# Performance work log

Measured on AMD Instinct MI355X. Metric: run time of the kernel, lower is better.

Reference implementation:

```python
import jax, jax.numpy as jnp
import numpy as np

NUM_SAMPLES = 4_194_304  # 2**22 samples (~87s @ 48kHz) -> memory-bound streaming IIR


def setup_inputs() -> dict:
    key = jax.random.key(0)
    k1, k2 = jax.random.split(key)
    # [attack, decay, filter_lp, filter_hp, gain]; uniform(0,1) is in the valid clamped range
    parameters = jax.random.uniform(k1, (5,), dtype=jnp.float32)
    noise = jax.random.normal(k2, (NUM_SAMPLES,), dtype=jnp.float32)
    return {"parameters": parameters, "noise": noise}


def _one_pole_lowpass(x, c):
    # y[n] = (1 - c) * x[n] + c * y[n-1]
    def step(y_prev, xn):
        y = (1.0 - c) * xn + c * y_prev
        return y, y
    _, y = jax.lax.scan(step, jnp.zeros((), x.dtype), x)
    return y


def _one_pole_highpass(x, c):
    # y[n] = c * (y[n-1] + x[n] - x[n-1])
    dx = jnp.concatenate([x[:1], x[1:] - x[:-1]])
    def step(y_prev, d):
        y = c * (y_prev + d)
        return y, y
    _, y = jax.lax.scan(step, jnp.zeros((), x.dtype), dx)
    return y


def reference(parameters, noise):
    attack = jnp.clip(parameters[0], 1e-7, None)
    decay = jnp.clip(parameters[1], 1e-7, None)
    filter_lp = jnp.clip(parameters[2], 1e-7, 0.99)
    filter_hp = jnp.clip(parameters[3], 1e-7, 0.99)
    gain = jnp.clip(parameters[4], 1e-7, None)

    n = noise.shape[0]
    t = jnp.linspace(0.0, 1.0, n, dtype=noise.dtype)  # matches registered 'time' buffer
    # exponential attack/decay envelope
    envelope = (1.0 - jnp.exp(-t / attack)) * jnp.exp(-t / decay)

    filtered = _one_pole_lowpass(noise, filter_lp)
    filtered = _one_pole_highpass(filtered, filter_hp)
    return filtered * envelope * gain
```

## Files before the change

kernel.cpp:

```cpp
#include <hip/hip_runtime.h>
#include <math.h>


#define BLOCK 256
#define CHUNK 16
#define SAMP  (BLOCK * CHUNK)
#define ESTG_CAP 4096

typedef float vfloat4 __attribute__((ext_vector_type(4)));
typedef float vfloat2 __attribute__((ext_vector_type(2)));

__device__ float Est_g[ESTG_CAP];

struct Op { float a, w, b; };
__device__ __forceinline__ Op opmul(Op A, Op B) {
    Op C;
    C.a = A.a * B.a;
    C.w = fmaf(A.w, B.a, A.b * B.w);
    C.b = A.b * B.b;
    return C;
}

template<bool EMIT>
__global__ __launch_bounds__(BLOCK, 4) void ng_kernel(
    const float* __restrict__ params,
    const float* __restrict__ noise,
    float* __restrict__ out,
    float* __restrict__ EstArg,
    int n)
{
    __shared__ float swy[4], swz[4], ry[4], rz[4];

    float* __restrict__ Est = EstArg ? EstArg : Est_g;

    const int tid  = threadIdx.x;
    const int lane = tid & 63;
    const int wid  = tid >> 6;
    const int b    = blockIdx.x;
    const int g0   = b * SAMP + tid * CHUNK;

    const float a   = fminf(fmaxf(params[2], 1e-7f), 0.99f);
    const float bb  = fminf(fmaxf(params[3], 1e-7f), 0.99f);
    const float omc = 1.0f - a;

    int nt = 0;
    vfloat2 Ev[4] = {{0.f,0.f},{0.f,0.f},{0.f,0.f},{0.f,0.f}};
    if (EMIT) {
        int em = b - 1 - tid;
        nt = (em >= 0) ? ((em >> 8) + 1) : 0;
        #pragma unroll
        for (int j = 0; j < 4; ++j) {
            if (j < nt) {
                int u = b - 1 - tid - (j << 8);
                Ev[j] = *(const vfloat2*)(Est + 2 * u);
            }
        }
    }

    vfloat4 xq[4];
    if (g0 + CHUNK <= n) {
        #pragma unroll
        for (int q = 0; q < 4; ++q)
            xq[q] = *(const vfloat4*)(noise + g0 + 4 * q);
    } else {
        #pragma unroll
        for (int q = 0; q < 4; ++q) {
            #pragma unroll
            for (int c = 0; c < 4; ++c) {
                int g = g0 + 4 * q + c;
                xq[q][c] = (g < n) ? noise[g] : 0.0f;
            }
        }
    }

    float yv = 0.0f, zv = 0.0f;
    #pragma unroll
    for (int j = 0; j < CHUNK; ++j) {
        float x  = xq[j >> 2][j & 3];
        float yn = fmaf(a, yv, omc * x);
        zv = bb * (zv + (yn - yv));
        yv = yn;
    }

    Op m1 = { a, bb * (a - 1.0f), bb };
    Op m2 = opmul(m1, m1), m4 = opmul(m2, m2), m8 = opmul(m4, m4);
    Op P  = opmul(m8, m8);
    Op O  = { 1.0f, 0.0f, 1.0f };
    float cy = yv, cz = zv;
    #pragma unroll
    for (int k = 0; k < 6; ++k) {
        if (EMIT && ((lane >> k) & 1)) O = opmul(P, O);
        int d = 1 << k;
        float py = __shfl_up(cy, d, 64);
        float pz = __shfl_up(cz, d, 64);
        if (lane >= d) {
            cy = fmaf(P.a, py, cy);
            cz = fmaf(P.w, py, fmaf(P.b, pz, cz));
        }
        P = opmul(P, P);
    }
    if (lane == 63) { swy[wid] = cy; swz[wid] = cz; }
    __syncthreads();

    float pry = 0.0f, prz = 0.0f;
    for (int u = 0; u < wid; ++u) {
        float ny = fmaf(P.a, pry, swy[u]);
        float nz = fmaf(P.w, pry, fmaf(P.b, prz, swz[u]));
        pry = ny; prz = nz;
    }

    if (!EMIT) {
        if (tid == 255) {
            vfloat2 e;
            e.x = fmaf(P.a, pry, cy);
            e.y = fmaf(P.w, pry, fmaf(P.b, prz, cz));
            *(vfloat2*)(Est + 2 * b) = e;
        }
        return;
    }

    float ey = __shfl_up(cy, 1, 64);
    float ez = __shfl_up(cz, 1, 64);
    if (lane == 0) { ey = 0.0f; ez = 0.0f; }

    Op R2 = opmul(P, P);
    Op Q  = opmul(R2, R2);
    Op Ot = { 1.0f, 0.0f, 1.0f };
    Op cur = Q;
    #pragma unroll
    for (int k = 0; k < 8; ++k) {
        if ((tid >> k) & 1) Ot = opmul(cur, Ot);
        cur = opmul(cur, cur);
    }
    float Hy = 0.0f, Hz = 0.0f;
    for (int j = nt - 1; j >= 4; --j) {
        int u = b - 1 - tid - (j << 8);
        vfloat2 e = *(const vfloat2*)(Est + 2 * u);
        float t = fmaf(cur.a, Hy, e.x);
        Hz = fmaf(cur.w, Hy, fmaf(cur.b, Hz, e.y));
        Hy = t;
    }
    #pragma unroll
    for (int j = 3; j >= 0; --j) {
        if (j < nt) {
            float t = fmaf(cur.a, Hy, Ev[j].x);
            Hz = fmaf(cur.w, Hy, fmaf(cur.b, Hz, Ev[j].y));
            Hy = t;
        }
    }
    float vy = Ot.a * Hy;
    float vz = fmaf(Ot.w, Hy, Ot.b * Hz);
    #pragma unroll
    for (int d = 1; d < 64; d <<= 1) {
        vy += __shfl_xor(vy, d, 64);
        vz += __shfl_xor(vz, d, 64);
    }
    if (lane == 0) { ry[wid] = vy; rz[wid] = vz; }
    __syncthreads();
    float s0y = (ry[0] + ry[1]) + (ry[2] + ry[3]);
    float s0z = (rz[0] + rz[1]) + (rz[2] + rz[3]);

    float wy = s0y, wz = s0z;
    for (int u = 0; u < wid; ++u) {
        float t = P.a * wy;
        wz = fmaf(P.w, wy, P.b * wz);
        wy = t;
    }
    wy += pry; wz += prz;
    float y0 = fmaf(O.a, wy, ey);
    float z0 = ez + fmaf(O.w, wy, O.b * wz);

    const float attack = fmaxf(params[0], 1e-7f);
    const float decay  = fmaxf(params[1], 1e-7f);
    const float gain   = fmaxf(params[4], 1e-7f);
    const float inv    = 1.0f / (float)(n - 1);
    const float ia = -1.0f / attack;
    const float id = -1.0f / decay;
    const float t0 = (float)g0 * inv;
    float ea = __expf(ia * t0);
    float ed = __expf(id * t0) * gain;
    const float ra = __expf(ia * inv);
    const float rd = __expf(id * inv);

    vfloat4 oq[4];
    yv = y0; zv = z0;
    #pragma unroll
    for (int j = 0; j < CHUNK; ++j) {
        float x  = xq[j >> 2][j & 3];
        float yn = fmaf(a, yv, omc * x);
        zv = bb * (zv + (yn - yv));
        yv = yn;
        oq[j >> 2][j & 3] = zv * ((1.0f - ea) * ed);
        ea *= ra; ed *= rd;
    }
    if (g0 + CHUNK <= n) {
        #pragma unroll
        for (int q = 0; q < 4; ++q)
            *(vfloat4*)(out + g0 + 4 * q) = oq[q];
    } else {
        #pragma unroll
        for (int q = 0; q < 4; ++q) {
            #pragma unroll
            for (int c = 0; c < 4; ++c) {
                int g = g0 + 4 * q + c;
                if (g < n) out[g] = oq[q][c];
            }
        }
    }
}

extern "C" void kernel_launch(void* const* d_in, const int* in_sizes, int n_in,
                              void* d_out, int out_size, void* d_ws, size_t ws_size,
                              hipStream_t stream) {
    const float* params = (const float*)d_in[0];
    const float* noise  = (const float*)d_in[1];
    float* out = (float*)d_out;
    int n = in_sizes[1];
    int grid = (n + SAMP - 1) / SAMP;
    float* Est = (ws_size >= (size_t)(2 * grid) * sizeof(float))
                     ? (float*)d_ws : nullptr;
    ng_kernel<false><<<grid, BLOCK, 0, stream>>>(params, noise, out, Est, n);
    ng_kernel<true ><<<grid, BLOCK, 0, stream>>>(params, noise, out, Est, n);
}
```

Measured before the change: 80.54 us.

## Fuse two-pass scan into one cooperative kernel with grid sync

Replaces the two-launch scheme (block-totals pass, then full recompute pass) with a single cooperative kernel. Each block publishes its carry, does a grid-wide sync, then folds in the prefix. The local zero-state filter outputs are kept in registers so the second pass only adds the homogeneous response, avoiding a second read of the noise and a second launch. The cost is a grid barrier that requires all 1024 blocks to be co-resident, with the old two-kernel path kept as a fallback if the cooperative launch fails.

```diff
diff --git a/kernel.cpp b/kernel.cpp
--- a/kernel.cpp
+++ b/kernel.cpp
@@ -1,4 +1,5 @@
 #include <hip/hip_runtime.h>
+#include <hip/hip_cooperative_groups.h>
 #include <math.h>
 
 
@@ -9,6 +10,8 @@
 
 typedef float vfloat4 __attribute__((ext_vector_type(4)));
 typedef float vfloat2 __attribute__((ext_vector_type(2)));
+
+namespace cg = cooperative_groups;
 
 __device__ float Est_g[ESTG_CAP];
 
@@ -21,8 +24,7 @@
     return C;
 }
 
-template<bool EMIT>
-__global__ __launch_bounds__(BLOCK, 4) void ng_kernel(
+__global__ __launch_bounds__(BLOCK, 4) void ng_coop(
     const float* __restrict__ params,
     const float* __restrict__ noise,
     float* __restrict__ out,
@@ -30,7 +32,6 @@
     int n)
 {
     __shared__ float swy[4], swz[4], ry[4], rz[4];
-
     float* __restrict__ Est = EstArg ? EstArg : Est_g;
 
     const int tid  = threadIdx.x;
@@ -42,20 +43,6 @@
     const float a   = fminf(fmaxf(params[2], 1e-7f), 0.99f);
     const float bb  = fminf(fmaxf(params[3], 1e-7f), 0.99f);
     const float omc = 1.0f - a;
-
-    int nt = 0;
-    vfloat2 Ev[4] = {{0.f,0.f},{0.f,0.f},{0.f,0.f},{0.f,0.f}};
-    if (EMIT) {
-        int em = b - 1 - tid;
-        nt = (em >= 0) ? ((em >> 8) + 1) : 0;
-        #pragma unroll
-        for (int j = 0; j < 4; ++j) {
-            if (j < nt) {
-                int u = b - 1 - tid - (j << 8);
-                Ev[j] = *(const vfloat2*)(Est + 2 * u);
-            }
-        }
-    }
 
     vfloat4 xq[4];
     if (g0 + CHUNK <= n) {
@@ -80,6 +67,7 @@
         float yn = fmaf(a, yv, omc * x);
         zv = bb * (zv + (yn - yv));
         yv = yn;
+        xq[j >> 2][j & 3] = zv;
     }
 
     Op m1 = { a, bb * (a - 1.0f), bb };
@@ -89,7 +77,7 @@
     float cy = yv, cz = zv;
     #pragma unroll
     for (int k = 0; k < 6; ++k) {
-        if (EMIT && ((lane >> k) & 1)) O = opmul(P, O);
+        if ((lane >> k) & 1) O = opmul(P, O);
         int d = 1 << k;
         float py = __shfl_up(cy, d, 64);
         float pz = __shfl_up(cz, d, 64);
@@ -109,20 +97,29 @@
         pry = ny; prz = nz;
     }
 
-    if (!EMIT) {
-        if (tid == 255) {
-            vfloat2 e;
-            e.x = fmaf(P.a, pry, cy);
-            e.y = fmaf(P.w, pry, fmaf(P.b, prz, cz));
-            *(vfloat2*)(Est + 2 * b) = e;
-        }
-        return;
-    }
-
     float ey = __shfl_up(cy, 1, 64);
     float ez = __shfl_up(cz, 1, 64);
     if (lane == 0) { ey = 0.0f; ez = 0.0f; }
 
+    if (tid == 255) {
+        vfloat2 e;
+        e.x = fmaf(P.a, pry, cy);
+        e.y = fmaf(P.w, pry, fmaf(P.b, prz, cz));
+        *(vfloat2*)(Est + 2 * b) = e;
+    }
+    __threadfence();
+    cg::this_grid().sync();
+
+    int em = b - 1 - tid;
+    int nt = (em >= 0) ? ((em >> 8) + 1) : 0;
+    vfloat2 Ev[4] = {{0.f,0.f},{0.f,0.f},{0.f,0.f},{0.f,0.f}};
+    #pragma unroll
+    for (int j = 0; j < 4; ++j) {
+        if (j < nt) {
+            int u = b - 1 - tid - (j << 8);
+            Ev[j] = *(const vfloat2*)(Est + 2 * u);
+        }
+    }
     Op R2 = opmul(P, P);
     Op Q  = opmul(R2, R2);
     Op Ot = { 1.0f, 0.0f, 1.0f };
@@ -167,8 +164,8 @@
         wy = t;
     }
     wy += pry; wz += prz;
-    float y0 = fmaf(O.a, wy, ey);
-    float z0 = ez + fmaf(O.w, wy, O.b * wz);
+    float yh = fmaf(O.a, wy, ey);
+    float zh = ez + fmaf(O.w, wy, O.b * wz);
 
     const float attack = fmaxf(params[0], 1e-7f);
     const float decay  = fmaxf(params[1], 1e-7f);
@@ -182,6 +179,191 @@
     const float ra = __expf(ia * inv);
     const float rd = __expf(id * inv);
 
+    #pragma unroll
+    for (int j = 0; j < CHUNK; ++j) {
+        float yn = a * yh;
+        zh = bb * (zh + (yn - yh));
+        yh = yn;
+        float zt = xq[j >> 2][j & 3] + zh;
+        xq[j >> 2][j & 3] = zt * ((1.0f - ea) * ed);
+        ea *= ra; ed *= rd;
+    }
+    if (g0 + CHUNK <= n) {
+        #pragma unroll
+        for (int q = 0; q < 4; ++q)
+            *(vfloat4*)(out + g0 + 4 * q) = xq[q];
+    } else {
+        #pragma unroll
+        for (int q = 0; q < 4; ++q) {
+            #pragma unroll
+            for (int c = 0; c < 4; ++c) {
+                int g = g0 + 4 * q + c;
+                if (g < n) out[g] = xq[q][c];
+            }
+        }
+    }
+}
+
+template<bool EMIT>
+__global__ __launch_bounds__(BLOCK, 4) void ng_kernel(
+    const float* __restrict__ params,
+    const float* __restrict__ noise,
+    float* __restrict__ out,
+    float* __restrict__ EstArg,
+    int n)
+{
+    __shared__ float swy[4], swz[4], ry[4], rz[4];
+    float* __restrict__ Est = EstArg ? EstArg : Est_g;
+
+    const int tid  = threadIdx.x;
+    const int lane = tid & 63;
+    const int wid  = tid >> 6;
+    const int b    = blockIdx.x;
+    const int g0   = b * SAMP + tid * CHUNK;
+
+    const float a   = fminf(fmaxf(params[2], 1e-7f), 0.99f);
+    const float bb  = fminf(fmaxf(params[3], 1e-7f), 0.99f);
+    const float omc = 1.0f - a;
+
+    int nt = 0;
+    vfloat2 Ev[4] = {{0.f,0.f},{0.f,0.f},{0.f,0.f},{0.f,0.f}};
+    if (EMIT) {
+        int em = b - 1 - tid;
+        nt = (em >= 0) ? ((em >> 8) + 1) : 0;
+        #pragma unroll
+        for (int j = 0; j < 4; ++j) {
+            if (j < nt) {
+                int u = b - 1 - tid - (j << 8);
+                Ev[j] = *(const vfloat2*)(Est + 2 * u);
+            }
+        }
+    }
+
+    vfloat4 xq[4];
+    if (g0 + CHUNK <= n) {
+        #pragma unroll
+        for (int q = 0; q < 4; ++q)
+            xq[q] = *(const vfloat4*)(noise + g0 + 4 * q);
+    } else {
+        #pragma unroll
+        for (int q = 0; q < 4; ++q) {
+            #pragma unroll
+            for (int c = 0; c < 4; ++c) {
+                int g = g0 + 4 * q + c;
+                xq[q][c] = (g < n) ? noise[g] : 0.0f;
+            }
+        }
+    }
+
+    float yv = 0.0f, zv = 0.0f;
+    #pragma unroll
+    for (int j = 0; j < CHUNK; ++j) {
+        float x  = xq[j >> 2][j & 3];
+        float yn = fmaf(a, yv, omc * x);
+        zv = bb * (zv + (yn - yv));
+        yv = yn;
+    }
+
+    Op m1 = { a, bb * (a - 1.0f), bb };
+    Op m2 = opmul(m1, m1), m4 = opmul(m2, m2), m8 = opmul(m4, m4);
+    Op P  = opmul(m8, m8);
+    Op O  = { 1.0f, 0.0f, 1.0f };
+    float cy = yv, cz = zv;
+    #pragma unroll
+    for (int k = 0; k < 6; ++k) {
+        if (EMIT && ((lane >> k) & 1)) O = opmul(P, O);
+        int d = 1 << k;
+        float py = __shfl_up(cy, d, 64);
+        float pz = __shfl_up(cz, d, 64);
+        if (lane >= d) {
+            cy = fmaf(P.a, py, cy);
+            cz = fmaf(P.w, py, fmaf(P.b, pz, cz));
+        }
+        P = opmul(P, P);
+    }
+    if (lane == 63) { swy[wid] = cy; swz[wid] = cz; }
+    __syncthreads();
+
+    float pry = 0.0f, prz = 0.0f;
+    for (int u = 0; u < wid; ++u) {
+        float ny = fmaf(P.a, pry, swy[u]);
+        float nz = fmaf(P.w, pry, fmaf(P.b, prz, swz[u]));
+        pry = ny; prz = nz;
+    }
+
+    if (!EMIT) {
+        if (tid == 255) {
+            vfloat2 e;
+            e.x = fmaf(P.a, pry, cy);
+            e.y = fmaf(P.w, pry, fmaf(P.b, prz, cz));
+            *(vfloat2*)(Est + 2 * b) = e;
+        }
+        return;
+    }
+
+    float ey = __shfl_up(cy, 1, 64);
+    float ez = __shfl_up(cz, 1, 64);
+    if (lane == 0) { ey = 0.0f; ez = 0.0f; }
+
+    Op R2 = opmul(P, P);
+    Op Q  = opmul(R2, R2);
+    Op Ot = { 1.0f, 0.0f, 1.0f };
+    Op cur = Q;
+    #pragma unroll
+    for (int k = 0; k < 8; ++k) {
+        if ((tid >> k) & 1) Ot = opmul(cur, Ot);
+        cur = opmul(cur, cur);
+    }
+    float Hy = 0.0f, Hz = 0.0f;
+    for (int j = nt - 1; j >= 4; --j) {
+        int u = b - 1 - tid - (j << 8);
+        vfloat2 e = *(const vfloat2*)(Est + 2 * u);
+        float t = fmaf(cur.a, Hy, e.x);
+        Hz = fmaf(cur.w, Hy, fmaf(cur.b, Hz, e.y));
+        Hy = t;
+    }
+    #pragma unroll
+    for (int j = 3; j >= 0; --j) {
+        if (j < nt) {
+            float t = fmaf(cur.a, Hy, Ev[j].x);
+            Hz = fmaf(cur.w, Hy, fmaf(cur.b, Hz, Ev[j].y));
+            Hy = t;
+        }
+    }
+    float vy = Ot.a * Hy;
+    float vz = fmaf(Ot.w, Hy, Ot.b * Hz);
+    #pragma unroll
+    for (int d = 1; d < 64; d <<= 1) {
+        vy += __shfl_xor(vy, d, 64);
+        vz += __shfl_xor(vz, d, 64);
+    }
+    if (lane == 0) { ry[wid] = vy; rz[wid] = vz; }
+    __syncthreads();
+    float s0y = (ry[0] + ry[1]) + (ry[2] + ry[3]);
+    float s0z = (rz[0] + rz[1]) + (rz[2] + rz[3]);
+
+    float wy = s0y, wz = s0z;
+    for (int u = 0; u < wid; ++u) {
+        float t = P.a * wy;
+        wz = fmaf(P.w, wy, P.b * wz);
+        wy = t;
+    }
+    wy += pry; wz += prz;
+    float y0 = fmaf(O.a, wy, ey);
+    float z0 = ez + fmaf(O.w, wy, O.b * wz);
+
+    const float attack = fmaxf(params[0], 1e-7f);
+    const float decay  = fmaxf(params[1], 1e-7f);
+    const float gain   = fmaxf(params[4], 1e-7f);
+    const float inv    = 1.0f / (float)(n - 1);
+    const float ia = -1.0f / attack;
+    const float id = -1.0f / decay;
+    const float t0 = (float)g0 * inv;
+    float ea = __expf(ia * t0);
+    float ed = __expf(id * t0) * gain;
+    const float ra = __expf(ia * inv);
+    const float rd = __expf(id * inv);
+
     vfloat4 oq[4];
     yv = y0; zv = z0;
     #pragma unroll
@@ -219,6 +401,14 @@
     int grid = (n + SAMP - 1) / SAMP;
     float* Est = (ws_size >= (size_t)(2 * grid) * sizeof(float))
                      ? (float*)d_ws : nullptr;
-    ng_kernel<false><<<grid, BLOCK, 0, stream>>>(params, noise, out, Est, n);
-    ng_kernel<true ><<<grid, BLOCK, 0, stream>>>(params, noise, out, Est, n);
+
+    void* args[] = { (void*)&params, (void*)&noise, (void*)&out,
+                     (void*)&Est, (void*)&n };
+    hipError_t err = hipLaunchCooperativeKernel(
+        reinterpret_cast<void*>(ng_coop), dim3(grid), dim3(BLOCK),
+        args, 0, stream);
+    if (err != hipSuccess) {
+        ng_kernel<false><<<grid, BLOCK, 0, stream>>>(params, noise, out, Est, n);
+        ng_kernel<true ><<<grid, BLOCK, 0, stream>>>(params, noise, out, Est, n);
+    }
 }
```

Result: slower. 264.4 us (+228.3%).
